# Performance work log

Measured on AMD Instinct MI355X. Metric: run time of the kernel, lower is better.

The kernel has to match this reference:

```python
import jax, jax.numpy as jnp
import numpy as np

B, S, D, H, L = 8, 1024, 768, 12, 8
DH = D // H
V, NCOND, DPA, NACT = 1024, 256, 64, 4
COND = DPA * NACT  # 256


def setup_inputs() -> dict:
    key = jax.random.key(0)
    ks = jax.random.split(key, 24)
    s = 0.02
    return {
        "tokens": jax.random.randint(ks[0], (B, S), 0, V),
        "actions": jax.random.randint(ks[1], (B, NACT), 0, NCOND),
        "emb": jax.random.normal(ks[2], (V, D)) * s,
        "act_emb": jax.random.normal(ks[3], (NCOND, DPA)) * s,
        "ln1_g": jax.random.normal(ks[4], (L, COND, D)) * s,
        "ln1_b": jax.random.normal(ks[5], (L, COND, D)) * s,
        "Wq": jax.random.normal(ks[6], (L, H, DH, DH)) * s,
        "Wk": jax.random.normal(ks[7], (L, H, DH, DH)) * s,
        "Wv": jax.random.normal(ks[8], (L, H, DH, DH)) * s,
        "Wo": jax.random.normal(ks[9], (L, D, D)) * s,
        "bo": jnp.zeros((L, D)),
        "ln2_g": jax.random.normal(ks[10], (L, COND, D)) * s,
        "ln2_b": jax.random.normal(ks[11], (L, COND, D)) * s,
        "W1": jax.random.normal(ks[12], (L, D, 4 * D)) * s,
        "b1": jnp.zeros((L, 4 * D)),
        "W2": jax.random.normal(ks[13], (L, 4 * D, D)) * s,
        "b2": jnp.zeros((L, D)),
        "lnf_g": jax.random.normal(ks[14], (COND, D)) * s,
        "lnf_b": jax.random.normal(ks[15], (COND, D)) * s,
        "Wout": jax.random.normal(ks[16], (D, V)) * s,
        "bout": jnp.zeros((V,)),
    }


def _sinusoidal_pe():
    pos = jnp.arange(S, dtype=jnp.float32)[:, None]
    div = jnp.exp(jnp.arange(0, D, 2, dtype=jnp.float32) * (-np.log(10000.0) / D))
    pe = jnp.zeros((S, D))
    pe = pe.at[:, 0::2].set(jnp.sin(pos * div))
    pe = pe.at[:, 1::2].set(jnp.cos(pos * div))
    return pe


def _cond_ln(x, a, gw, bw, eps=1e-5):
    # affine-free layernorm, conditional gain/shift from action vector (VideoGPT-style CondLayerNorm)
    mu = x.mean(-1, keepdims=True)
    var = ((x - mu) ** 2).mean(-1, keepdims=True)
    h = (x - mu) * jax.lax.rsqrt(var + eps)
    g = a @ gw  # [B, D]
    b = a @ bw
    return h * g[:, None, :] + b[:, None, :]


def _attn(h, wq, wk, wv, wo, bo_):
    xh = h.reshape(B, S, H, DH)
    q = jnp.einsum("bshd,hde->bshe", xh, wq)
    k = jnp.einsum("bshd,hde->bshe", xh, wk)
    v = jnp.einsum("bshd,hde->bshe", xh, wv)
    logits = jnp.einsum("bshe,bthe->bhst", q, k) / np.sqrt(DH)  # d_model per head = DH
    p = jax.nn.softmax(logits, axis=-1)
    o = jnp.einsum("bhst,bthd->bshd", p, v).reshape(B, S, D)
    return o @ wo + bo_


def reference(tokens, actions, emb, act_emb, ln1_g, ln1_b, Wq, Wk, Wv, Wo, bo,
              ln2_g, ln2_b, W1, b1, W2, b2, lnf_g, lnf_b, Wout, bout):
    x = emb[tokens] + _sinusoidal_pe()[None]  # [B, S, D]
    a = act_emb[actions].reshape(B, -1)  # first_action_only -> [B, COND]
    for l in range(L):
        h = _cond_ln(x, a, ln1_g[l], ln1_b[l])
        x = x + _attn(h, Wq[l], Wk[l], Wv[l], Wo[l], bo[l])
        h = _cond_ln(x, a, ln2_g[l], ln2_b[l])
        h = jax.nn.gelu(h @ W1[l] + b1[l]) @ W2[l] + b2[l]
        x = x + h
    x = _cond_ln(x, a, lnf_g, lnf_b)
    return x @ Wout + bout
```

## Files before the change

### kernel.cpp

```cpp
#include <hip/hip_runtime.h>
#include <hip/hip_bf16.h>

typedef unsigned short u16;
typedef __attribute__((ext_vector_type(8))) short bf16x8;
typedef __attribute__((ext_vector_type(4))) float f32x4;

#define NB 8
#define NS 1024
#define ND 768
#define NH 12
#define NL 8
#define NDH 64
#define NV 1024
#define NCONDV 256
#define NTOK (NB*NS)

union BF8 { bf16x8 v; u16 u[8]; };
union US4 { ushort4 v; u16 u[4]; };

__device__ __forceinline__ float b2f(u16 u){ return __uint_as_float(((unsigned)u) << 16); }
__device__ __forceinline__ u16 f2b(float f){
  unsigned u = __float_as_uint(f);
  return (u16)((u + 0x7fffu + ((u >> 16) & 1u)) >> 16);
}

__device__ __forceinline__ void glds16(const u16* g, u16* l) {
  __builtin_amdgcn_global_load_lds((const __attribute__((address_space(1))) void*)g,
                                   (__attribute__((address_space(3))) void*)l, 16, 0, 0);
}

#define MEMFENCE asm volatile("" ::: "memory")

__global__ __launch_bounds__(256) void k_embed(const int* __restrict__ tokens,
                                               const float* __restrict__ emb,
                                               float* __restrict__ x)
{
  const int t = blockIdx.x;
  const int s = t & (NS - 1);
  const int tok = tokens[t];
  const float c = (float)(-9.210340371976184 / 768.0);
  for (int d = threadIdx.x; d < ND; d += 256) {
    float div = expf((float)(d & ~1) * c);
    float ang = (float)s * div;
    float pe = (d & 1) ? cosf(ang) : sinf(ang);
    x[(size_t)t*ND + d] = emb[(size_t)tok*ND + d] + pe;
  }
}

__global__ __launch_bounds__(256) void k_actvec(const int* __restrict__ actions,
                                                const float* __restrict__ act_emb,
                                                float* __restrict__ a)
{
  const int b = blockIdx.x, j = threadIdx.x;
  const int i = j >> 6, kk = j & 63;
  const int act = actions[b*4 + i];
  a[b*NCONDV + j] = act_emb[(size_t)act*64 + kk];
}

__global__ __launch_bounds__(256) void k_gains(const float* __restrict__ a,
    const float* __restrict__ g1, const float* __restrict__ b1,
    const float* __restrict__ g2, const float* __restrict__ b2,
    const float* __restrict__ gf, const float* __restrict__ bfp,
    float* __restrict__ outp)
{
  __shared__ float sa[NB*NCONDV];
  const int m = blockIdx.x, dc = blockIdx.y;
  for (int i = threadIdx.x; i < NB*NCONDV; i += 256) sa[i] = a[i];
  __syncthreads();
  const float* W;
  if (m < 32) {
    int ll = m >> 2, w = m & 3;
    const float* base = (w==0) ? g1 : (w==1) ? b1 : (w==2) ? g2 : b2;
    W = base + (size_t)ll * NCONDV * ND;
  } else {
    W = (m == 32) ? gf : bfp;
  }
  const int d = dc*256 + threadIdx.x;
  float acc[NB] = {0,0,0,0,0,0,0,0};
  for (int j = 0; j < NCONDV; j++) {
    float w = W[(size_t)j*ND + d];
    #pragma unroll
    for (int bb = 0; bb < NB; bb++) acc[bb] += sa[bb*NCONDV + j] * w;
  }
  #pragma unroll
  for (int bb = 0; bb < NB; bb++) outp[((size_t)m*NB + bb)*ND + d] = acc[bb];
}

__global__ __launch_bounds__(256) void k_cln(const float* __restrict__ x,
                                             const float* __restrict__ g,
                                             const float* __restrict__ bb,
                                             u16* __restrict__ h)
{
  const int tid = threadIdx.x, w = tid >> 6, lane = tid & 63;
  const int t = blockIdx.x*4 + w;
  const int bi = t >> 10;
  const float* xr = x + (size_t)t*ND;
  f32x4 v0 = *(const f32x4*)(xr + lane*4);
  f32x4 v1 = *(const f32x4*)(xr + 256 + lane*4);
  f32x4 v2 = *(const f32x4*)(xr + 512 + lane*4);
  float s = (v0[0]+v0[1]+v0[2]+v0[3]) + (v1[0]+v1[1]+v1[2]+v1[3]) + (v2[0]+v2[1]+v2[2]+v2[3]);
  #pragma unroll
  for (int off = 1; off < 64; off <<= 1) s += __shfl_xor(s, off);
  float mu = s * (1.0f/768.0f);
  float s2 = 0.f;
  #pragma unroll
  for (int i = 0; i < 4; i++) { v0[i] -= mu; s2 += v0[i]*v0[i]; }
  #pragma unroll
  for (int i = 0; i < 4; i++) { v1[i] -= mu; s2 += v1[i]*v1[i]; }
  #pragma unroll
  for (int i = 0; i < 4; i++) { v2[i] -= mu; s2 += v2[i]*v2[i]; }
  #pragma unroll
  for (int off = 1; off < 64; off <<= 1) s2 += __shfl_xor(s2, off);
  float rs = rsqrtf(s2 * (1.0f/768.0f) + 1e-5f);
  const float* gr = g + (size_t)bi*ND;
  const float* br = bb + (size_t)bi*ND;
  u16* hr = h + (size_t)t*ND;
  #pragma unroll
  for (int j = 0; j < 3; j++) {
    f32x4 vv = (j==0) ? v0 : (j==1) ? v1 : v2;
    f32x4 gg = *(const f32x4*)(gr + j*256 + lane*4);
    f32x4 bv = *(const f32x4*)(br + j*256 + lane*4);
    US4 o;
    #pragma unroll
    for (int i = 0; i < 4; i++) o.u[i] = f2b(vv[i]*rs*gg[i] + bv[i]);
    *(ushort4*)(hr + j*256 + lane*4) = o.v;
  }
}

__global__ __launch_bounds__(256) void k_wprep(const float* __restrict__ src,
                                               u16* __restrict__ dst, int K, int N)
{
  __shared__ u16 t[64][65];
  const int k0 = blockIdx.x*64, n0 = blockIdx.y*64;
  const size_t mz = (size_t)blockIdx.z * K * N;
  src += mz; dst += mz;
  {
    int r = threadIdx.x >> 2, c0 = (threadIdx.x & 3) * 16;
    const float* s = src + (size_t)(k0 + r)*N + n0 + c0;
    f32x4 a = *(const f32x4*)s, b = *(const f32x4*)(s+4);
    f32x4 c = *(const f32x4*)(s+8), d = *(const f32x4*)(s+12);
    #pragma unroll
    for (int i = 0; i < 4; i++) {
      t[r][c0+i]    = f2b(a[i]);
      t[r][c0+4+i]  = f2b(b[i]);
      t[r][c0+8+i]  = f2b(c[i]);
      t[r][c0+12+i] = f2b(d[i]);
    }
  }
  __syncthreads();
  {
    int rn = threadIdx.x >> 2, kc = (threadIdx.x & 3)*16;
    u16* dp = dst + (size_t)(n0+rn)*K + k0 + kc;
    BF8 o0, o1;
    #pragma unroll
    for (int i = 0; i < 8; i++) { o0.u[i] = t[kc+i][rn]; o1.u[i] = t[kc+8+i][rn]; }
    *(bf16x8*)dp = o0.v; *(bf16x8*)(dp+8) = o1.v;
  }
}

__global__ __launch_bounds__(256) void k_qkv(const u16* __restrict__ h,
    const float* __restrict__ Wq, const float* __restrict__ Wk, const float* __restrict__ Wv,
    u16* __restrict__ qo, u16* __restrict__ ko, u16* __restrict__ vo)
{
  __shared__ alignas(16) u16 wlds[3][64][72];
  const int t0 = blockIdx.x * 64, head = blockIdx.y;
  {
    int d = threadIdx.x >> 2, e0 = (threadIdx.x & 3) * 16;
    #pragma unroll
    for (int which = 0; which < 3; which++) {
      const float* W = ((which==0) ? Wq : (which==1) ? Wk : Wv) + (size_t)head*NDH*NDH;
      const float* wr = W + (size_t)d*NDH + e0;
      f32x4 f0 = *(const f32x4*)wr;
      f32x4 f1 = *(const f32x4*)(wr + 4);
      f32x4 f2 = *(const f32x4*)(wr + 8);
      f32x4 f3 = *(const f32x4*)(wr + 12);
      #pragma unroll
      for (int i = 0; i < 4; i++) {
        wlds[which][e0+i][d]    = f2b(f0[i]);
        wlds[which][e0+4+i][d]  = f2b(f1[i]);
        wlds[which][e0+8+i][d]  = f2b(f2[i]);
        wlds[which][e0+12+i][d] = f2b(f3[i]);
      }
    }
  }
  __syncthreads();
  const int wave = threadIdx.x >> 6, lane = threadIdx.x & 63;
  const int lo16 = lane & 15, quad = lane >> 4;
  const int arow = t0 + wave*16 + lo16;
  const u16* hr = h + (size_t)arow*ND + head*NDH + quad*8;
  bf16x8 a0 = *(const bf16x8*)hr;
  bf16x8 a1 = *(const bf16x8*)(hr + 32);
  #pragma unroll
  for (int which = 0; which < 3; which++) {
    f32x4 acc[4] = {{0,0,0,0},{0,0,0,0},{0,0,0,0},{0,0,0,0}};
    #pragma unroll
    for (int n = 0; n < 4; n++) {
      const u16* bp = &wlds[which][n*16 + lo16][quad*8];
      bf16x8 b0 = *(const bf16x8*)bp;
      bf16x8 b1 = *(const bf16x8*)(bp + 32);
      acc[n] = __builtin_amdgcn_mfma_f32_16x16x32_bf16(a0, b0, acc[n], 0, 0, 0);
      acc[n] = __builtin_amdgcn_mfma_f32_16x16x32_bf16(a1, b1, acc[n], 0, 0, 0);
    }
    #pragma unroll
    for (int n = 0; n < 4; n++) {
      #pragma unroll
      for (int r = 0; r < 4; r++) {
        int t = t0 + wave*16 + quad*4 + r;
        int bb = t >> 10, s = t & (NS-1);
        int e = n*16 + lo16;
        u16 val = f2b(acc[n][r]);
        if (which == 2) {
          int local = s & 127;
          int col = (s & ~127) | (((local & 15) << 3) | (local >> 4));
          vo[(((size_t)bb*NH + head)*NDH + e)*NS + col] = val;
        } else {
          u16* dst = (which == 0) ? qo : ko;
          dst[(((size_t)bb*NH + head)*NS + s)*NDH + e] = val;
        }
      }
    }
  }
}

__global__ __launch_bounds__(256) void k_attn2(const u16* __restrict__ q,
                                               const u16* __restrict__ kk,
                                               const u16* __restrict__ vt,
                                               u16* __restrict__ o)
{
  __shared__ alignas(16) u16 klds[128][72];
  __shared__ alignas(16) u16 vlds[64][136];
  __shared__ alignas(16) u16 plds[4][16][136];
  const int tid = threadIdx.x, w = tid >> 6, lane = tid & 63;
  const int lo16 = lane & 15, quad = lane >> 4;
  const int bh = blockIdx.x;
  const int b = bh / NH, head = bh - b*NH;
  const int q0 = blockIdx.y*64 + w*16;
  const u16* qb = q  + (size_t)bh*NS*NDH;
  const u16* kb = kk + (size_t)bh*NS*NDH;
  const u16* vb = vt + (size_t)bh*NDH*NS;
  BF8 aq0, aq1;
  {
    const u16* qr = qb + (size_t)(q0 + lo16)*NDH + quad*8;
    BF8 r0, r1; r0.v = *(const bf16x8*)qr; r1.v = *(const bf16x8*)(qr + 32);
    const float qs = 0.125f * 1.44269504088896f;
    #pragma unroll
    for (int j = 0; j < 8; j++) {
      aq0.u[j] = f2b(b2f(r0.u[j]) * qs);
      aq1.u[j] = f2b(b2f(r1.u[j]) * qs);
    }
  }
  float lsum[4] = {0,0,0,0};
  f32x4 oacc[4] = {{0,0,0,0},{0,0,0,0},{0,0,0,0},{0,0,0,0}};

  bf16x8 kreg[4], vreg[4];
  #pragma unroll
  for (int i = 0; i < 4; i++) {
    int c = tid + 256*i;
    kreg[i] = *(const bf16x8*)(kb + (size_t)(c>>3)*NDH + (c&7)*8);
    vreg[i] = *(const bf16x8*)(vb + (size_t)(c>>4)*NS + (c&15)*8);
  }

  for (int kt = 0; kt < NS; kt += 128) {
    __syncthreads();
    #pragma unroll
    for (int i = 0; i < 4; i++) {
      int c = tid + 256*i;
      *(bf16x8*)&klds[c>>3][(c&7)*8] = kreg[i];
      *(bf16x8*)&vlds[c>>4][(c&15)*8] = vreg[i];
    }
    __syncthreads();
    if (kt + 128 < NS) {
      #pragma unroll
      for (int i = 0; i < 4; i++) {
        int c = tid + 256*i;
        kreg[i] = *(const bf16x8*)(kb + (size_t)(kt + 128 + (c>>3))*NDH + (c&7)*8);
        vreg[i] = *(const bf16x8*)(vb + (size_t)(c>>4)*NS + (kt + 128) + (c&15)*8);
      }
    }
    f32x4 s[8];
    #pragma unroll
    for (int j = 0; j < 8; j++) {
      const u16* kr = &klds[j*16 + lo16][quad*8];
      bf16x8 b0 = *(const bf16x8*)kr;
      bf16x8 b1 = *(const bf16x8*)(kr + 32);
      f32x4 z = {0,0,0,0};
      z = __builtin_amdgcn_mfma_f32_16x16x32_bf16(aq0.v, b0, z, 0, 0, 0);
      s[j] = __builtin_amdgcn_mfma_f32_16x16x32_bf16(aq1.v, b1, z, 0, 0, 0);
    }
    #pragma unroll
    for (int r = 0; r < 4; r++) {
      float p[8];
      #pragma unroll
      for (int j = 0; j < 8; j++) p[j] = exp2f(s[j][r]);
      unsigned pk32[4];
      #pragma unroll
      for (int j = 0; j < 4; j++)
        asm("v_cvt_pk_bf16_f32 %0, %1, %2" : "=v"(pk32[j]) : "v"(p[2*j]), "v"(p[2*j+1]));
      float ps = 0.f;
      #pragma unroll
      for (int j = 0; j < 4; j++) {
        ps += __uint_as_float(pk32[j] << 16);
        ps += __uint_as_float(pk32[j] & 0xffff0000u);
      }
      lsum[r] += ps;
      union { unsigned u[4]; bf16x8 v; } pkv;
      #pragma unroll
      for (int j = 0; j < 4; j++) pkv.u[j] = pk32[j];
      *(bf16x8*)&plds[w][quad*4 + r][lo16*8] = pkv.v;
    }
    #pragma unroll
    for (int kc = 0; kc < 4; kc++) {
      bf16x8 pa = *(const bf16x8*)&plds[w][lo16][kc*32 + quad*8];
      #pragma unroll
      for (int n = 0; n < 4; n++) {
        bf16x8 vf = *(const bf16x8*)&vlds[n*16 + lo16][kc*32 + quad*8];
        oacc[n] = __builtin_amdgcn_mfma_f32_16x16x32_bf16(pa, vf, oacc[n], 0, 0, 0);
      }
    }
  }
  #pragma unroll
  for (int r = 0; r < 4; r++) {
    #pragma unroll
    for (int off = 1; off < 16; off <<= 1) lsum[r] += __shfl_xor(lsum[r], off);
  }
  #pragma unroll
  for (int n = 0; n < 4; n++) {
    #pragma unroll
    for (int r = 0; r < 4; r++) {
      int s_ = q0 + quad*4 + r;
      int d = head*NDH + n*16 + lo16;
      o[((size_t)b*NS + s_)*ND + d] = f2b(oacc[n][r] / lsum[r]);
    }
  }
}

template<int EPI>
__global__ __launch_bounds__(256) void k_gemm6(
    const u16* __restrict__ A, const u16* __restrict__ Bt,
    const float* __restrict__ bias, const float* __restrict__ resid,
    void* __restrict__ out, int M, int N, int K)
{
  __shared__ alignas(16) u16 lds[2*16384];
  const int tid = threadIdx.x;
  const int lane = tid & 63, lo16 = lane & 15, quad = lane >> 4;
  const int w = tid >> 6;
  const int wm = (w & 1) << 6;
  const int wn = (w >> 1) << 6;

  const int nwg = (int)gridDim.x, flat = (int)blockIdx.x;
  const int swzid = ((nwg & 7) == 0) ? ((flat & 7) * (nwg >> 3) + (flat >> 3)) : flat;
  const int nbn = N >> 7;
  const int mb = swzid / nbn, nb = swzid - mb*nbn;
  const int m0 = mb << 7, n0 = nb << 7;
  const int NT = K >> 6;

  const int sr = tid >> 3, ss = tid & 7;
  const int sg = ((ss ^ (sr & 7)) << 3);
  const u16* Asrc = A + (size_t)(m0 + sr) * K + sg;
  const u16* Bsrc = Bt + (size_t)(n0 + sr) * K + sg;
  const size_t K32 = (size_t)K << 5;
  u16* const sd = lds + tid * 8;

  const int sw0 = ((quad ^ (lo16 & 7)) << 3);
  const int sw1 = (((4 + quad) ^ (lo16 & 7)) << 3);
  const int arow = (wm + lo16) << 6;
  const int brow = (wn + lo16) << 6;

  float bv[4];
  #pragma unroll
  for (int nf = 0; nf < 4; nf++) {
    bv[nf] = bias[n0 + wn + nf*16 + lo16];
    asm volatile("" :: "v"(bv[nf]));
  }

  f32x4 acc[4][4];
  #pragma unroll
  for (int i = 0; i < 4; i++)
    #pragma unroll
    for (int j = 0; j < 4; j++) acc[i][j] = (f32x4){0,0,0,0};

  auto STAGE = [&](int t, int bi) {
    u16* dst = sd + bi * 16384;
    const size_t ko = (size_t)t << 6;
    #pragma unroll
    for (int c = 0; c < 4; c++) glds16(Asrc + ko + (size_t)c*K32, dst + c*2048);
    #pragma unroll
    for (int c = 0; c < 4; c++) glds16(Bsrc + ko + (size_t)c*K32, dst + 8192 + c*2048);
  };

  STAGE(0, 0);
  for (int t = 0; t < NT; t++) {
    MEMFENCE; __builtin_amdgcn_s_barrier(); MEMFENCE;
    if (t + 1 < NT) {
      STAGE(t + 1, (t + 1) & 1);
      asm volatile("s_waitcnt vmcnt(8)" ::: "memory");
    } else {
      asm volatile("s_waitcnt vmcnt(0)" ::: "memory");
    }
    MEMFENCE; __builtin_amdgcn_s_barrier(); MEMFENCE;
    const u16* cb = lds + (t & 1) * 16384;
    bf16x8 af[4][2], bf[4][2];
    #pragma unroll
    for (int mf = 0; mf < 4; mf++) {
      af[mf][0] = *(const bf16x8*)(cb + arow + mf*1024 + sw0);
      af[mf][1] = *(const bf16x8*)(cb + arow + mf*1024 + sw1);
    }
    #pragma unroll
    for (int nf = 0; nf < 4; nf++) {
      bf[nf][0] = *(const bf16x8*)(cb + 8192 + brow + nf*1024 + sw0);
      bf[nf][1] = *(const bf16x8*)(cb + 8192 + brow + nf*1024 + sw1);
    }
    __builtin_amdgcn_s_setprio(1);
    #pragma unroll
    for (int kk = 0; kk < 2; kk++)
      #pragma unroll
      for (int mf = 0; mf < 4; mf++)
        #pragma unroll
        for (int nf = 0; nf < 4; nf++)
          acc[mf][nf] = __builtin_amdgcn_mfma_f32_16x16x32_bf16(af[mf][kk], bf[nf][kk], acc[mf][nf], 0, 0, 0);
    __builtin_amdgcn_s_setprio(0);
  }

  #pragma unroll
  for (int mf = 0; mf < 4; mf++) {
    #pragma unroll
    for (int nf = 0; nf < 4; nf++) {
      const int col = n0 + wn + nf*16 + lo16;
      #pragma unroll
      for (int r = 0; r < 4; r++) {
        const int row = m0 + wm + mf*16 + quad*4 + r;
        const size_t idx = (size_t)row * N + col;
        float v = acc[mf][nf][r] + bv[nf];
        if (EPI == 1) {
          float u = 0.7978845608028654f*(v + 0.044715f*v*v*v);
          float e = __expf(2.0f*u);
          float th = (e - 1.0f) / (e + 1.0f);
          ((u16*)out)[idx] = f2b(0.5f*v*(1.0f + th));
        } else if (EPI == 2) {
          ((float*)out)[idx] = v + resid[idx];
        } else {
          ((float*)out)[idx] = v;
        }
      }
    }
  }
}

template<int EPI>
__global__ __launch_bounds__(256) void k_gemm7(
    const u16* __restrict__ A, const u16* __restrict__ Bt,
    const float* __restrict__ bias, const float* __restrict__ resid,
    void* __restrict__ out, int M, int N, int K)
{
  __shared__ alignas(16) u16 lds[2*12288];
  const int tid = threadIdx.x;
  const int lane = tid & 63, lo16 = lane & 15, quad = lane >> 4;
  const int w = tid >> 6;
  const int wm = (w & 1) << 5;
  const int wn = (w >> 1) << 6;

  const int nwg = (int)gridDim.x, flat = (int)blockIdx.x;
  const int swzid = ((nwg & 7) == 0) ? ((flat & 7) * (nwg >> 3) + (flat >> 3)) : flat;
  const int nbn = N >> 7;
  const int mb = swzid / nbn, nb = swzid - mb*nbn;
  const int m0 = mb << 6, n0 = nb << 7;
  const int NT = K >> 6;

  const int sr = tid >> 3, ss = tid & 7;
  const int sg = ((ss ^ (sr & 7)) << 3);
  const u16* Asrc = A + (size_t)(m0 + sr) * K + sg;
  const u16* Bsrc = Bt + (size_t)(n0 + sr) * K + sg;
  const size_t K32 = (size_t)K << 5;
  u16* const sd = lds + tid * 8;

  const int sw0 = ((quad ^ (lo16 & 7)) << 3);
  const int sw1 = (((4 + quad) ^ (lo16 & 7)) << 3);
  const int arow = (wm + lo16) << 6;
  const int brow = (wn + lo16) << 6;

  float bv[4];
  #pragma unroll
  for (int nf = 0; nf < 4; nf++) {
    bv[nf] = bias[n0 + wn + nf*16 + lo16];
    asm volatile("" :: "v"(bv[nf]));
  }

  f32x4 acc[2][4];
  #pragma unroll
  for (int i = 0; i < 2; i++)
    #pragma unroll
    for (int j = 0; j < 4; j++) acc[i][j] = (f32x4){0,0,0,0};

  auto STAGE = [&](int t, int bi) {
    u16* dst = sd + bi * 12288;
    const size_t ko = (size_t)t << 6;
    #pragma unroll
    for (int c = 0; c < 2; c++) glds16(Asrc + ko + (size_t)c*K32, dst + c*2048);
    #pragma unroll
    for (int c = 0; c < 4; c++) glds16(Bsrc + ko + (size_t)c*K32, dst + 4096 + c*2048);
  };

  STAGE(0, 0);
  for (int t = 0; t < NT; t++) {
    MEMFENCE; __builtin_amdgcn_s_barrier(); MEMFENCE;
    if (t + 1 < NT) {
      STAGE(t + 1, (t + 1) & 1);
      asm volatile("s_waitcnt vmcnt(6)" ::: "memory");
    } else {
      asm volatile("s_waitcnt vmcnt(0)" ::: "memory");
    }
    MEMFENCE; __builtin_amdgcn_s_barrier(); MEMFENCE;
    const u16* cb = lds + (t & 1) * 12288;
    bf16x8 af[2][2], bf[4][2];
    #pragma unroll
    for (int mf = 0; mf < 2; mf++) {
      af[mf][0] = *(const bf16x8*)(cb + arow + mf*1024 + sw0);
      af[mf][1] = *(const bf16x8*)(cb + arow + mf*1024 + sw1);
    }
    #pragma unroll
    for (int nf = 0; nf < 4; nf++) {
      bf[nf][0] = *(const bf16x8*)(cb + 4096 + brow + nf*1024 + sw0);
      bf[nf][1] = *(const bf16x8*)(cb + 4096 + brow + nf*1024 + sw1);
    }
    __builtin_amdgcn_s_setprio(1);
    #pragma unroll
    for (int kk = 0; kk < 2; kk++)
      #pragma unroll
      for (int mf = 0; mf < 2; mf++)
        #pragma unroll
        for (int nf = 0; nf < 4; nf++)
          acc[mf][nf] = __builtin_amdgcn_mfma_f32_16x16x32_bf16(af[mf][kk], bf[nf][kk], acc[mf][nf], 0, 0, 0);
    __builtin_amdgcn_s_setprio(0);
  }

  #pragma unroll
  for (int mf = 0; mf < 2; mf++) {
    #pragma unroll
    for (int nf = 0; nf < 4; nf++) {
      const int col = n0 + wn + nf*16 + lo16;
      #pragma unroll
      for (int r = 0; r < 4; r++) {
        const int row = m0 + wm + mf*16 + quad*4 + r;
        const size_t idx = (size_t)row * N + col;
        float v = acc[mf][nf][r] + bv[nf];
        if (EPI == 1) {
          float u = 0.7978845608028654f*(v + 0.044715f*v*v*v);
          float e = __expf(2.0f*u);
          float th = (e - 1.0f) / (e + 1.0f);
          ((u16*)out)[idx] = f2b(0.5f*v*(1.0f + th));
        } else if (EPI == 2) {
          ((float*)out)[idx] = v + resid[idx];
        } else {
          ((float*)out)[idx] = v;
        }
      }
    }
  }
}

template<int EPI>
__global__ __launch_bounds__(256) void k_gemm(
    const u16* __restrict__ A, const float* __restrict__ Bw,
    const float* __restrict__ bias, const float* resid,
    void* out, int M, int N, int K)
{
  __shared__ alignas(16) u16 alds[64][40];
  __shared__ alignas(16) u16 blds[64][40];
  const int m0 = blockIdx.x * 64, n0b = blockIdx.y * 64;
  const int tid = threadIdx.x;
  const int wave = tid >> 6, lane = tid & 63, lo16 = lane & 15, quad = lane >> 4;
  f32x4 acc[4] = {{0,0,0,0},{0,0,0,0},{0,0,0,0},{0,0,0,0}};
  const int ar = tid >> 2, ac = (tid & 3) * 8;
  const int bk = tid >> 3, bn = (tid & 7) * 8;
  for (int k0 = 0; k0 < K; k0 += 32) {
    __syncthreads();
    *(bf16x8*)&alds[ar][ac] = *(const bf16x8*)(A + (size_t)(m0+ar)*K + k0 + ac);
    {
      const float* brow = Bw + (size_t)(k0+bk)*N + n0b + bn;
      f32x4 f0 = *(const f32x4*)brow;
      f32x4 f1 = *(const f32x4*)(brow + 4);
      #pragma unroll
      for (int i = 0; i < 4; i++) {
        blds[bn+i][bk]   = f2b(f0[i]);
        blds[bn+4+i][bk] = f2b(f1[i]);
      }
    }
    __syncthreads();
    bf16x8 af = *(const bf16x8*)&alds[wave*16 + lo16][quad*8];
    #pragma unroll
    for (int n = 0; n < 4; n++) {
      bf16x8 bf = *(const bf16x8*)&blds[n*16 + lo16][quad*8];
      acc[n] = __builtin_amdgcn_mfma_f32_16x16x32_bf16(af, bf, acc[n], 0, 0, 0);
    }
  }
  const int rbase = m0 + wave*16 + quad*4;
  #pragma unroll
  for (int n = 0; n < 4; n++) {
    int col = n0b + n*16 + lo16;
    float bv = bias[col];
    #pragma unroll
    for (int r = 0; r < 4; r++) {
      int row = rbase + r;
      float v = acc[n][r] + bv;
      if (EPI == 1) {
        float x3 = v*v*v;
        v = 0.5f*v*(1.0f + tanhf(0.7978845608028654f*(v + 0.044715f*x3)));
        ((u16*)out)[(size_t)row*N + col] = f2b(v);
      } else if (EPI == 2) {
        ((float*)out)[(size_t)row*N + col] = v + resid[(size_t)row*N + col];
      } else {
        ((float*)out)[(size_t)row*N + col] = v;
      }
    }
  }
}

extern "C" void kernel_launch(void* const* d_in, const int* in_sizes, int n_in,
                              void* d_out, int out_size, void* d_ws, size_t ws_size,
                              hipStream_t stream)
{
  (void)in_sizes; (void)n_in; (void)out_size;
  const int*   tokens  = (const int*)d_in[0];
  const int*   actions = (const int*)d_in[1];
  const float* emb     = (const float*)d_in[2];
  const float* act_emb = (const float*)d_in[3];
  const float* ln1_g   = (const float*)d_in[4];
  const float* ln1_b   = (const float*)d_in[5];
  const float* Wq      = (const float*)d_in[6];
  const float* Wk      = (const float*)d_in[7];
  const float* Wv      = (const float*)d_in[8];
  const float* Wo      = (const float*)d_in[9];
  const float* bo      = (const float*)d_in[10];
  const float* ln2_g   = (const float*)d_in[11];
  const float* ln2_b   = (const float*)d_in[12];
  const float* W1      = (const float*)d_in[13];
  const float* b1      = (const float*)d_in[14];
  const float* W2      = (const float*)d_in[15];
  const float* b2      = (const float*)d_in[16];
  const float* lnf_g   = (const float*)d_in[17];
  const float* lnf_b   = (const float*)d_in[18];
  const float* Wout    = (const float*)d_in[19];
  const float* bout    = (const float*)d_in[20];

  char* p = (char*)d_ws;
  float* abuf = (float*)p;  p += (size_t)NB*NCONDV*4;
  float* gbuf = (float*)p;  p += (size_t)34*NB*ND*4;
  float* xbuf = (float*)p;  p += (size_t)NTOK*ND*4;
  u16*   hbuf = (u16*)p;    p += (size_t)NTOK*ND*2;
  u16*   region = (u16*)p;
  u16* qbuf = region;
  u16* kbuf = region + (size_t)NTOK*ND;
  u16* vbuf = region + (size_t)2*NTOK*ND;
  u16* obuf = (u16*)d_out;

  size_t base = (size_t)(p - (char*)d_ws) + (size_t)3*NTOK*ND*2;
  size_t hid_sz = (size_t)NTOK*3072*2;
  size_t woT_sz = (size_t)NL*ND*ND*2;
  size_t w1T_sz = (size_t)NL*ND*3072*2;
  size_t w2T_sz = (size_t)NL*3072*ND*2;
  size_t woutT_sz = (size_t)ND*NV*2;
  size_t req_fast = base + hid_sz + woT_sz + w1T_sz + w2T_sz + woutT_sz;
  const bool fast = (ws_size >= req_fast);

  k_embed <<<NTOK, 256, 0, stream>>>(tokens, emb, xbuf);
  k_actvec<<<NB, 256, 0, stream>>>(actions, act_emb, abuf);
  k_gains <<<dim3(34,3), 256, 0, stream>>>(abuf, ln1_g, ln1_b, ln2_g, ln2_b, lnf_g, lnf_b, gbuf);

  if (fast) {
    char* q2 = (char*)d_ws + base;
    u16* hidbuf = (u16*)q2;  q2 += hid_sz;
    u16* WoT   = (u16*)q2;   q2 += woT_sz;
    u16* W1T   = (u16*)q2;   q2 += w1T_sz;
    u16* W2T   = (u16*)q2;   q2 += w2T_sz;
    u16* WoutT = (u16*)q2;

    k_wprep<<<dim3(ND/64, ND/64, NL), 256, 0, stream>>>(Wo, WoT, ND, ND);
    k_wprep<<<dim3(ND/64, 3072/64, NL), 256, 0, stream>>>(W1, W1T, ND, 3072);
    k_wprep<<<dim3(3072/64, ND/64, NL), 256, 0, stream>>>(W2, W2T, 3072, ND);
    k_wprep<<<dim3(ND/64, NV/64, 1), 256, 0, stream>>>(Wout, WoutT, ND, NV);

    for (int l = 0; l < NL; l++) {
      k_cln<<<NTOK/4, 256, 0, stream>>>(xbuf, gbuf + (size_t)(l*4+0)*NB*ND, gbuf + (size_t)(l*4+1)*NB*ND, hbuf);
      k_qkv<<<dim3(NTOK/64, NH), 256, 0, stream>>>(hbuf,
          Wq + (size_t)l*NH*NDH*NDH, Wk + (size_t)l*NH*NDH*NDH, Wv + (size_t)l*NH*NDH*NDH,
          qbuf, kbuf, vbuf);
      k_attn2<<<dim3(NB*NH, NS/64), 256, 0, stream>>>(qbuf, kbuf, vbuf, obuf);
      k_gemm7<2><<<dim3((NTOK/64)*(ND/128)), 256, 0, stream>>>(
          obuf, WoT + (size_t)l*ND*ND, bo + (size_t)l*ND, xbuf, xbuf, NTOK, ND, ND);
      k_cln<<<NTOK/4, 256, 0, stream>>>(xbuf, gbuf + (size_t)(l*4+2)*NB*ND, gbuf + (size_t)(l*4+3)*NB*ND, hbuf);
      k_gemm6<1><<<dim3((NTOK/128)*(3072/128)), 256, 0, stream>>>(
          hbuf, W1T + (size_t)l*ND*3072, b1 + (size_t)l*3072, nullptr, hidbuf, NTOK, 3072, ND);
      k_gemm7<2><<<dim3((NTOK/64)*(ND/128)), 256, 0, stream>>>(
          hidbuf, W2T + (size_t)l*3072*ND, b2 + (size_t)l*ND, xbuf, xbuf, NTOK, ND, 3072);
    }
    k_cln<<<NTOK/4, 256, 0, stream>>>(xbuf, gbuf + (size_t)32*NB*ND, gbuf + (size_t)33*NB*ND, hbuf);
    k_gemm6<0><<<dim3((NTOK/128)*(NV/128)), 256, 0, stream>>>(
        hbuf, WoutT, bout, nullptr, (float*)d_out, NTOK, NV, ND);
  } else {
    u16* hidbuf = region;
    for (int l = 0; l < NL; l++) {
      k_cln<<<NTOK/4, 256, 0, stream>>>(xbuf, gbuf + (size_t)(l*4+0)*NB*ND, gbuf + (size_t)(l*4+1)*NB*ND, hbuf);
      k_qkv<<<dim3(NTOK/64, NH), 256, 0, stream>>>(hbuf,
          Wq + (size_t)l*NH*NDH*NDH, Wk + (size_t)l*NH*NDH*NDH, Wv + (size_t)l*NH*NDH*NDH,
          qbuf, kbuf, vbuf);
      k_attn2<<<dim3(NB*NH, NS/64), 256, 0, stream>>>(qbuf, kbuf, vbuf, obuf);
      k_gemm<2><<<dim3(NTOK/64, ND/64), 256, 0, stream>>>(obuf, Wo + (size_t)l*ND*ND,
          bo + (size_t)l*ND, xbuf, xbuf, NTOK, ND, ND);
      k_cln<<<NTOK/4, 256, 0, stream>>>(xbuf, gbuf + (size_t)(l*4+2)*NB*ND, gbuf + (size_t)(l*4+3)*NB*ND, hbuf);
      for (int c = 0; c < 2; c++) {
        const size_t mo = (size_t)c * 4096;
        k_gemm<1><<<dim3(4096/64, 3072/64), 256, 0, stream>>>(hbuf + mo*ND, W1 + (size_t)l*ND*3072,
            b1 + (size_t)l*3072, nullptr, hidbuf, 4096, 3072, ND);
        k_gemm<2><<<dim3(4096/64, ND/64), 256, 0, stream>>>(hidbuf, W2 + (size_t)l*3072*ND,
            b2 + (size_t)l*ND, xbuf + mo*ND, xbuf + mo*ND, 4096, ND, 3072);
      }
    }
    k_cln<<<NTOK/4, 256, 0, stream>>>(xbuf, gbuf + (size_t)32*NB*ND, gbuf + (size_t)33*NB*ND, hbuf);
    k_gemm<0><<<dim3(NTOK/64, NV/64), 256, 0, stream>>>(hbuf, Wout, bout, nullptr, (float*)d_out, NTOK, NV, ND);
  }
}
```

Baseline: 2.225 ms.

## Replace gemm7 with 128x128 BK=32 gemm8 and reassign GEMM kernels per layer

```diff
diff --git a/kernel.cpp b/kernel.cpp
--- a/kernel.cpp
+++ b/kernel.cpp
@@ -447,36 +447,35 @@
 }
 
 template<int EPI>
-__global__ __launch_bounds__(256) void k_gemm7(
+__global__ __launch_bounds__(256) void k_gemm8(
     const u16* __restrict__ A, const u16* __restrict__ Bt,
     const float* __restrict__ bias, const float* __restrict__ resid,
     void* __restrict__ out, int M, int N, int K)
 {
-  __shared__ alignas(16) u16 lds[2*12288];
+  __shared__ alignas(16) u16 lds[2*8192];
   const int tid = threadIdx.x;
   const int lane = tid & 63, lo16 = lane & 15, quad = lane >> 4;
   const int w = tid >> 6;
-  const int wm = (w & 1) << 5;
+  const int wm = (w & 1) << 6;
   const int wn = (w >> 1) << 6;
 
   const int nwg = (int)gridDim.x, flat = (int)blockIdx.x;
   const int swzid = ((nwg & 7) == 0) ? ((flat & 7) * (nwg >> 3) + (flat >> 3)) : flat;
   const int nbn = N >> 7;
   const int mb = swzid / nbn, nb = swzid - mb*nbn;
-  const int m0 = mb << 6, n0 = nb << 7;
-  const int NT = K >> 6;
-
-  const int sr = tid >> 3, ss = tid & 7;
-  const int sg = ((ss ^ (sr & 7)) << 3);
+  const int m0 = mb << 7, n0 = nb << 7;
+  const int NT = K >> 5;
+
+  const int sr = tid >> 2, ss = tid & 3;
+  const int sg = ((ss ^ ((sr >> 1) & 3)) << 3);
   const u16* Asrc = A + (size_t)(m0 + sr) * K + sg;
   const u16* Bsrc = Bt + (size_t)(n0 + sr) * K + sg;
-  const size_t K32 = (size_t)K << 5;
+  const size_t K64r = (size_t)K << 6;
   u16* const sd = lds + tid * 8;
 
-  const int sw0 = ((quad ^ (lo16 & 7)) << 3);
-  const int sw1 = (((4 + quad) ^ (lo16 & 7)) << 3);
-  const int arow = (wm + lo16) << 6;
-  const int brow = (wn + lo16) << 6;
+  const int swr = ((quad ^ ((lo16 >> 1) & 3)) << 3);
+  const int arow = (wm + lo16) << 5;
+  const int brow = (wn + lo16) << 5;
 
   float bv[4];
   #pragma unroll
@@ -485,19 +484,19 @@
     asm volatile("" :: "v"(bv[nf]));
   }
 
-  f32x4 acc[2][4];
-  #pragma unroll
-  for (int i = 0; i < 2; i++)
+  f32x4 acc[4][4];
+  #pragma unroll
+  for (int i = 0; i < 4; i++)
     #pragma unroll
     for (int j = 0; j < 4; j++) acc[i][j] = (f32x4){0,0,0,0};
 
   auto STAGE = [&](int t, int bi) {
-    u16* dst = sd + bi * 12288;
-    const size_t ko = (size_t)t << 6;
-    #pragma unroll
-    for (int c = 0; c < 2; c++) glds16(Asrc + ko + (size_t)c*K32, dst + c*2048);
-    #pragma unroll
-    for (int c = 0; c < 4; c++) glds16(Bsrc + ko + (size_t)c*K32, dst + 4096 + c*2048);
+    u16* dst = sd + bi * 8192;
+    const size_t ko = (size_t)t << 5;
+    glds16(Asrc + ko,        dst);
+    glds16(Asrc + ko + K64r, dst + 2048);
+    glds16(Bsrc + ko,        dst + 4096);
+    glds16(Bsrc + ko + K64r, dst + 4096 + 2048);
   };
 
   STAGE(0, 0);
@@ -505,36 +504,30 @@
     MEMFENCE; __builtin_amdgcn_s_barrier(); MEMFENCE;
     if (t + 1 < NT) {
       STAGE(t + 1, (t + 1) & 1);
-      asm volatile("s_waitcnt vmcnt(6)" ::: "memory");
+      asm volatile("s_waitcnt vmcnt(4)" ::: "memory");
     } else {
       asm volatile("s_waitcnt vmcnt(0)" ::: "memory");
     }
     MEMFENCE; __builtin_amdgcn_s_barrier(); MEMFENCE;
-    const u16* cb = lds + (t & 1) * 12288;
-    bf16x8 af[2][2], bf[4][2];
-    #pragma unroll
-    for (int mf = 0; mf < 2; mf++) {
-      af[mf][0] = *(const bf16x8*)(cb + arow + mf*1024 + sw0);
-      af[mf][1] = *(const bf16x8*)(cb + arow + mf*1024 + sw1);
-    }
-    #pragma unroll
-    for (int nf = 0; nf < 4; nf++) {
-      bf[nf][0] = *(const bf16x8*)(cb + 4096 + brow + nf*1024 + sw0);
-      bf[nf][1] = *(const bf16x8*)(cb + 4096 + brow + nf*1024 + sw1);
-    }
+    const u16* cb = lds + (t & 1) * 8192;
+    bf16x8 af[4], bf[4];
+    #pragma unroll
+    for (int mf = 0; mf < 4; mf++)
+      af[mf] = *(const bf16x8*)(cb + arow + mf*512 + swr);
+    #pragma unroll
+    for (int nf = 0; nf < 4; nf++)
+      bf[nf] = *(const bf16x8*)(cb + 4096 + brow + nf*512 + swr);
     __builtin_amdgcn_s_setprio(1);
     #pragma unroll
-    for (int kk = 0; kk < 2; kk++)
-      #pragma unroll
-      for (int mf = 0; mf < 2; mf++)
-        #pragma unroll
-        for (int nf = 0; nf < 4; nf++)
-          acc[mf][nf] = __builtin_amdgcn_mfma_f32_16x16x32_bf16(af[mf][kk], bf[nf][kk], acc[mf][nf], 0, 0, 0);
+    for (int mf = 0; mf < 4; mf++)
+      #pragma unroll
+      for (int nf = 0; nf < 4; nf++)
+        acc[mf][nf] = __builtin_amdgcn_mfma_f32_16x16x32_bf16(af[mf], bf[nf], acc[mf][nf], 0, 0, 0);
     __builtin_amdgcn_s_setprio(0);
   }
 
   #pragma unroll
-  for (int mf = 0; mf < 2; mf++) {
+  for (int mf = 0; mf < 4; mf++) {
     #pragma unroll
     for (int nf = 0; nf < 4; nf++) {
       const int col = n0 + wn + nf*16 + lo16;
@@ -685,16 +678,16 @@
           Wq + (size_t)l*NH*NDH*NDH, Wk + (size_t)l*NH*NDH*NDH, Wv + (size_t)l*NH*NDH*NDH,
           qbuf, kbuf, vbuf);
       k_attn2<<<dim3(NB*NH, NS/64), 256, 0, stream>>>(qbuf, kbuf, vbuf, obuf);
-      k_gemm7<2><<<dim3((NTOK/64)*(ND/128)), 256, 0, stream>>>(
+      k_gemm6<2><<<dim3((NTOK/128)*(ND/128)), 256, 0, stream>>>(
           obuf, WoT + (size_t)l*ND*ND, bo + (size_t)l*ND, xbuf, xbuf, NTOK, ND, ND);
       k_cln<<<NTOK/4, 256, 0, stream>>>(xbuf, gbuf + (size_t)(l*4+2)*NB*ND, gbuf + (size_t)(l*4+3)*NB*ND, hbuf);
-      k_gemm6<1><<<dim3((NTOK/128)*(3072/128)), 256, 0, stream>>>(
+      k_gemm8<1><<<dim3((NTOK/128)*(3072/128)), 256, 0, stream>>>(
           hbuf, W1T + (size_t)l*ND*3072, b1 + (size_t)l*3072, nullptr, hidbuf, NTOK, 3072, ND);
-      k_gemm7<2><<<dim3((NTOK/64)*(ND/128)), 256, 0, stream>>>(
+      k_gemm6<2><<<dim3((NTOK/128)*(ND/128)), 256, 0, stream>>>(
           hidbuf, W2T + (size_t)l*3072*ND, b2 + (size_t)l*ND, xbuf, xbuf, NTOK, ND, 3072);
     }
     k_cln<<<NTOK/4, 256, 0, stream>>>(xbuf, gbuf + (size_t)32*NB*ND, gbuf + (size_t)33*NB*ND, hbuf);
-    k_gemm6<0><<<dim3((NTOK/128)*(NV/128)), 256, 0, stream>>>(
+    k_gemm8<0><<<dim3((NTOK/128)*(NV/128)), 256, 0, stream>>>(
         hbuf, WoutT, bout, nullptr, (float*)d_out, NTOK, NV, ND);
   } else {
     u16* hidbuf = region;
```

After: 2.182 ms. About the same (-2.0%).
